# Performance work log

Measured on AMD Instinct MI355X. Metric: run time of the kernel, lower is better.

## Reference

```python
import jax, jax.numpy as jnp
import numpy as np

B, C, H, W = 32, 3, 128, 128
OH, OW = 32, 32
N = OH * OW


def calc_mask(mu_x, mu_y, sigma_x, sigma_y):
    # Gaussian receptive-field mask, normalized per neuron over (C,H,W) and
    # rescaled by sqrt(C*H*W), as in AdaptiveLocal2DLayer.calc_U (channel_separate=False,
    # normed=True). The mask is identical across channels, so we keep it [H,W,N]
    # and fold the channel count C into the normalization.
    xg = jnp.linspace(0.0, 1.0, W)
    yg = jnp.linspace(0.0, 1.0, H)
    gx = jnp.exp(-0.5 * ((xg[:, None] - mu_x[None, :]) / sigma_x[None, :]) ** 2)  # [W,N]
    gy = jnp.exp(-0.5 * ((yg[:, None] - mu_y[None, :]) / sigma_y[None, :]) ** 2)  # [H,N]
    g = gy[:, None, :] * gx[None, :, :]  # [H,W,N]
    sumsq = C * jnp.sum(g * g, axis=(0, 1), keepdims=True)  # per-neuron sum over C,H,W
    return g / jnp.sqrt(sumsq) * jnp.sqrt(jnp.asarray(C * H * W, dtype=g.dtype))


def setup_inputs() -> dict:
    key = jax.random.key(0)
    kx, kw = jax.random.split(key)
    x = jax.random.normal(kx, (B, C, H, W), dtype=jnp.float32)
    # mu_init='spread': grid of centers with margin 0.2 (np.meshgrid default 'xy')
    margin = 0.2
    grid_y, grid_x = jnp.meshgrid(
        jnp.linspace(margin, 1.0 - margin, OH),
        jnp.linspace(margin, 1.0 - margin, OW),
        indexing='xy')
    mu_x = grid_x.flatten().astype(jnp.float32)
    mu_y = grid_y.flatten().astype(jnp.float32)
    sigma_x = jnp.full((N,), 0.1, dtype=jnp.float32)
    sigma_y = jnp.full((N,), 0.1, dtype=jnp.float32)
    # weight init as in the module: uniform(-bound, bound) with
    # bound = gain*sqrt(6/(eff_fan_in + fan_out)), eff_fan_in = sum(mask^2)
    mask = calc_mask(mu_x, mu_y, sigma_x, sigma_y)
    eff_fan_in = C * jnp.sum(mask ** 2)
    gain = float(np.sqrt(2.0))  # calculate_gain('relu')
    bound = gain * jnp.sqrt(6.0 / (eff_fan_in + N))
    weights = jax.random.uniform(kw, (C, H, W, N), minval=-bound, maxval=bound,
                                 dtype=jnp.float32)
    return {"x": x, "mu_x": mu_x, "mu_y": mu_y,
            "sigma_x": sigma_x, "sigma_y": sigma_y, "weights": weights}


def reference(x, mu_x, mu_y, sigma_x, sigma_y, weights):
    # forward: weighted_mask = mask * weights; tensordot over (C,H,W)
    mask = calc_mask(mu_x, mu_y, sigma_x, sigma_y)  # [H,W,N]
    wm = mask[None, :, :, :] * weights               # [C,H,W,N]
    out = jnp.einsum('bchw,chwn->bn', x, wm)         # [B,N]
    return out.reshape(x.shape[0], 1, OH, OW)
```

## Files before the change

kernel.cpp:

```cpp
#include <hip/hip_runtime.h>

#define BB 32
#define CC 3
#define HH 128
#define WW 128
#define NN 1024
#define KK (CC*HH*WW)
#define NROWS (CC*HH)
#define KSR NROWS
#define BH 16
#define BSPLIT (BB/BH)
#define WCH 4
#define NCH (WW/WCH)
#define SG 8
#define STEP (1.0f/127.0f)

__global__ void scale_kernel(const float* __restrict__ mu_x,
                             const float* __restrict__ mu_y,
                             const float* __restrict__ sigma_x,
                             const float* __restrict__ sigma_y,
                             float* __restrict__ scale) {
    int n = blockIdx.x * blockDim.x + threadIdx.x;
    if (n >= NN) return;
    float mux = mu_x[n], muy = mu_y[n];
    float isx = 1.0f / sigma_x[n], isy = 1.0f / sigma_y[n];
    float Sx = 0.f, Sy = 0.f;
    for (int i = 0; i < WW; ++i) {
        float dx = (i * STEP - mux) * isx;
        Sx += __expf(-dx * dx);
        float dy = (i * STEP - muy) * isy;
        Sy += __expf(-dy * dy);
    }
    scale[n] = sqrtf((float)(HH * WW) / (Sx * Sy));
}

__global__ void xpose_kernel(const float* __restrict__ x, float* __restrict__ xT) {
    __shared__ float tile[64][BB + 1];
    int k0 = blockIdx.x * 64;
    int lane = threadIdx.x & 63;
    int bgrp = threadIdx.x >> 6;
#pragma unroll
    for (int i = 0; i < 8; ++i) {
        int b = bgrp * 8 + i;
        tile[lane][b] = x[(size_t)b * KK + k0 + lane];
    }
    __syncthreads();
    int b = threadIdx.x & 31;
    int kk0 = threadIdx.x >> 5;
#pragma unroll
    for (int i = 0; i < 8; ++i) {
        int kk = i * 8 + kk0;
        xT[(size_t)(k0 + kk) * BB + b] = tile[kk][b];
    }
}

__global__ __launch_bounds__(256) void main_pipe(
    const float* __restrict__ weights,
    const float* __restrict__ xT,
    const float* __restrict__ scale,
    const float* __restrict__ mu_x, const float* __restrict__ mu_y,
    const float* __restrict__ sigma_x, const float* __restrict__ sigma_y,
    float* __restrict__ part)
{
    const int tid  = threadIdx.x;
    const int wv   = tid >> 6;
    const int lane = tid & 63;

    const int d    = blockIdx.x;
    const int xcd  = d & 7;
    const int slot = d >> 3;
    const int g    = xcd * (KSR / 8) + (slot >> 1);
    const int b0   = (slot & 1) * BH;
    const int r    = g;
    const int h    = r & (HH - 1);
    const int nq   = wv * 64 + lane;

    const float4 mux = ((const float4*)mu_x)[nq];
    const float4 sx4 = ((const float4*)sigma_x)[nq];
    const float4 muy = ((const float4*)mu_y)[nq];
    const float4 sy4 = ((const float4*)sigma_y)[nq];
    const float4 sc4 = ((const float4*)scale)[nq];

    float4 ax, axs, Bf, gyrow;
    ax.x = -0.5f/(sx4.x*sx4.x); ax.y = -0.5f/(sx4.y*sx4.y);
    ax.z = -0.5f/(sx4.z*sx4.z); ax.w = -0.5f/(sx4.w*sx4.w);
    axs.x = ax.x*STEP; axs.y = ax.y*STEP; axs.z = ax.z*STEP; axs.w = ax.w*STEP;
    Bf.x = __expf(2.f*axs.x*STEP); Bf.y = __expf(2.f*axs.y*STEP);
    Bf.z = __expf(2.f*axs.z*STEP); Bf.w = __expf(2.f*axs.w*STEP);
    {
        const float hp = h * STEP;
        float ayc, dd;
        ayc = -0.5f/(sy4.x*sy4.x); dd = hp-muy.x; gyrow.x = __expf(ayc*dd*dd)*sc4.x;
        ayc = -0.5f/(sy4.y*sy4.y); dd = hp-muy.y; gyrow.y = __expf(ayc*dd*dd)*sc4.y;
        ayc = -0.5f/(sy4.z*sy4.z); dd = hp-muy.z; gyrow.z = __expf(ayc*dd*dd)*sc4.z;
        ayc = -0.5f/(sy4.w*sy4.w); dd = hp-muy.w; gyrow.w = __expf(ayc*dd*dd)*sc4.w;
    }

    const float* wbase = weights + (size_t)r * WW * NN + nq * 4;
    const float4* xr4  = (const float4*)xT + (size_t)r * (WW * BB / 4) + (b0 >> 2);

    float4 wR[2][4];
#define WLOAD(BUF, C)                                                   \
    {                                                                   \
        _Pragma("unroll")                                               \
        for (int i = 0; i < 4; ++i)                                     \
            wR[BUF][i] = *(const float4*)(wbase + (size_t)((C)*WCH + i) * NN); \
    }

    float4 acc[BH];
#pragma unroll
    for (int b = 0; b < BH; ++b) acc[b] = make_float4(0.f, 0.f, 0.f, 0.f);

    float4 g4, r4;
    auto resync = [&](int w0) {
        const float w0s = (float)w0 * STEP;
        float dd;
        dd = w0s - mux.x; g4.x = __expf(ax.x*dd*dd)*gyrow.x; r4.x = __expf(axs.x*(2.f*dd+STEP));
        dd = w0s - mux.y; g4.y = __expf(ax.y*dd*dd)*gyrow.y; r4.y = __expf(axs.y*(2.f*dd+STEP));
        dd = w0s - mux.z; g4.z = __expf(ax.z*dd*dd)*gyrow.z; r4.z = __expf(axs.z*(2.f*dd+STEP));
        dd = w0s - mux.w; g4.w = __expf(ax.w*dd*dd)*gyrow.w; r4.w = __expf(axs.w*(2.f*dd+STEP));
    };

#define FMAQ(XQ, A0)                                                    \
    {                                                                   \
        acc[A0+0].x = fmaf(XQ.x, t.x, acc[A0+0].x);                     \
        acc[A0+0].y = fmaf(XQ.x, t.y, acc[A0+0].y);                     \
        acc[A0+0].z = fmaf(XQ.x, t.z, acc[A0+0].z);                     \
        acc[A0+0].w = fmaf(XQ.x, t.w, acc[A0+0].w);                     \
        acc[A0+1].x = fmaf(XQ.y, t.x, acc[A0+1].x);                     \
        acc[A0+1].y = fmaf(XQ.y, t.y, acc[A0+1].y);                     \
        acc[A0+1].z = fmaf(XQ.y, t.z, acc[A0+1].z);                     \
        acc[A0+1].w = fmaf(XQ.y, t.w, acc[A0+1].w);                     \
        acc[A0+2].x = fmaf(XQ.z, t.x, acc[A0+2].x);                     \
        acc[A0+2].y = fmaf(XQ.z, t.y, acc[A0+2].y);                     \
        acc[A0+2].z = fmaf(XQ.z, t.z, acc[A0+2].z);                     \
        acc[A0+2].w = fmaf(XQ.z, t.w, acc[A0+2].w);                     \
        acc[A0+3].x = fmaf(XQ.w, t.x, acc[A0+3].x);                     \
        acc[A0+3].y = fmaf(XQ.w, t.y, acc[A0+3].y);                     \
        acc[A0+3].z = fmaf(XQ.w, t.z, acc[A0+3].z);                     \
        acc[A0+3].w = fmaf(XQ.w, t.w, acc[A0+3].w);                     \
    }

#define CHUNK(BUF, C)                                                   \
    {                                                                   \
        if (((C) & 3) == 0) resync((C) * WCH);                          \
        _Pragma("unroll")                                               \
        for (int i = 0; i < 4; ++i) {                                   \
            const int w = (C) * WCH + i;                                \
            const float4 xq0 = xr4[w*8 + 0];                            \
            const float4 xq1 = xr4[w*8 + 1];                            \
            const float4 xq2 = xr4[w*8 + 2];                            \
            const float4 xq3 = xr4[w*8 + 3];                            \
            const float4 wt  = wR[BUF][i];                              \
            float4 t;                                                   \
            t.x = g4.x * wt.x; t.y = g4.y * wt.y;                       \
            t.z = g4.z * wt.z; t.w = g4.w * wt.w;                       \
            FMAQ(xq0, 0)                                                \
            FMAQ(xq1, 4)                                                \
            FMAQ(xq2, 8)                                                \
            FMAQ(xq3, 12)                                               \
            g4.x *= r4.x; g4.y *= r4.y; g4.z *= r4.z; g4.w *= r4.w;     \
            r4.x *= Bf.x; r4.y *= Bf.y; r4.z *= Bf.z; r4.w *= Bf.w;     \
        }                                                               \
    }

    WLOAD(0, 0);
    for (int c = 0; c < NCH; c += 2) {
        WLOAD(1, c + 1);
        CHUNK(0, c);
        if (c + 2 < NCH) WLOAD(0, c + 2);
        CHUNK(1, c + 1);
    }
#undef CHUNK
#undef FMAQ
#undef WLOAD

    float* pp = part + ((size_t)g * BB + b0) * NN + (tid << 2);
#pragma unroll
    for (int b = 0; b < BH; ++b)
        *(float4*)(pp + (size_t)b * NN) = acc[b];
}

__global__ __launch_bounds__(256) void reduce1_kernel(const float* __restrict__ part,
                                                      float* __restrict__ part2) {
    const int sg = blockIdx.x >> 5;
    const int cq = (blockIdx.x & 31) * 256 + threadIdx.x;
    const int s0 = sg * (KSR / SG);
    float4 a = make_float4(0.f, 0.f, 0.f, 0.f);
#pragma unroll 4
    for (int s = 0; s < KSR / SG; ++s) {
        const float4 v = *(const float4*)(part + (size_t)(s0 + s) * (BB * NN) + cq * 4);
        a.x += v.x; a.y += v.y; a.z += v.z; a.w += v.w;
    }
    *(float4*)(part2 + ((size_t)sg * (BB * NN) + cq * 4)) = a;
}

__global__ __launch_bounds__(256) void reduce2_kernel(const float* __restrict__ part2,
                                                      float* __restrict__ out) {
    const int cq = blockIdx.x * 256 + threadIdx.x;
    float4 a = make_float4(0.f, 0.f, 0.f, 0.f);
#pragma unroll
    for (int sgi = 0; sgi < SG; ++sgi) {
        const float4 v = *(const float4*)(part2 + (size_t)sgi * (BB * NN) + cq * 4);
        a.x += v.x; a.y += v.y; a.z += v.z; a.w += v.w;
    }
    *(float4*)(out + cq * 4) = a;
}

__global__ __launch_bounds__(256) void main_fallback(
    const float* __restrict__ weights,
    const float* __restrict__ x,
    const float* __restrict__ mu_x, const float* __restrict__ mu_y,
    const float* __restrict__ sigma_x, const float* __restrict__ sigma_y,
    float* __restrict__ dst)
{
    __shared__ float tile[2][WW][8];
    const int tid = threadIdx.x;
    const int g   = blockIdx.x;
    const int b0  = blockIdx.y * 8;
    const int r0  = g * 2;

    {
        const int b = tid & 7;
        const int c = tid >> 3;
        const float* xp = x + (size_t)(b0 + b) * KK + (size_t)r0 * WW + c * 8;
        const float4 v0 = ((const float4*)xp)[0];
        const float4 v1 = ((const float4*)xp)[1];
        const int row = (c * 8) >> 7;
        const int w   = (c * 8) & (WW - 1);
        tile[row][w+0][b] = v0.x; tile[row][w+1][b] = v0.y;
        tile[row][w+2][b] = v0.z; tile[row][w+3][b] = v0.w;
        tile[row][w+4][b] = v1.x; tile[row][w+5][b] = v1.y;
        tile[row][w+6][b] = v1.z; tile[row][w+7][b] = v1.w;
    }

    float4 mux4 = ((const float4*)mu_x)[tid];
    float4 muy4 = ((const float4*)mu_y)[tid];
    float4 sx4  = ((const float4*)sigma_x)[tid];
    float4 sy4  = ((const float4*)sigma_y)[tid];
    float4 ax4, ay4, sc4;
    ax4.x=-0.5f/(sx4.x*sx4.x); ax4.y=-0.5f/(sx4.y*sx4.y);
    ax4.z=-0.5f/(sx4.z*sx4.z); ax4.w=-0.5f/(sx4.w*sx4.w);
    ay4.x=-0.5f/(sy4.x*sy4.x); ay4.y=-0.5f/(sy4.y*sy4.y);
    ay4.z=-0.5f/(sy4.z*sy4.z); ay4.w=-0.5f/(sy4.w*sy4.w);
    {
        float Sx[4]={0,0,0,0}, Sy[4]={0,0,0,0};
        for (int i = 0; i < WW; ++i) {
            float pp = i * STEP, dd;
            dd=pp-mux4.x; Sx[0]+=__expf(2.f*ax4.x*dd*dd);
            dd=pp-mux4.y; Sx[1]+=__expf(2.f*ax4.y*dd*dd);
            dd=pp-mux4.z; Sx[2]+=__expf(2.f*ax4.z*dd*dd);
            dd=pp-mux4.w; Sx[3]+=__expf(2.f*ax4.w*dd*dd);
            dd=pp-muy4.x; Sy[0]+=__expf(2.f*ay4.x*dd*dd);
            dd=pp-muy4.y; Sy[1]+=__expf(2.f*ay4.y*dd*dd);
            dd=pp-muy4.z; Sy[2]+=__expf(2.f*ay4.z*dd*dd);
            dd=pp-muy4.w; Sy[3]+=__expf(2.f*ay4.w*dd*dd);
        }
        sc4.x = sqrtf((float)(HH*WW)/(Sx[0]*Sy[0]));
        sc4.y = sqrtf((float)(HH*WW)/(Sx[1]*Sy[1]));
        sc4.z = sqrtf((float)(HH*WW)/(Sx[2]*Sy[2]));
        sc4.w = sqrtf((float)(HH*WW)/(Sx[3]*Sy[3]));
    }
    __syncthreads();

    float acc[8][4];
#pragma unroll
    for (int b = 0; b < 8; ++b)
        acc[b][0] = acc[b][1] = acc[b][2] = acc[b][3] = 0.f;

#pragma unroll
    for (int rr = 0; rr < 2; ++rr) {
        const int rrow = r0 + rr;
        const int hh = rrow & (HH - 1);
        float4 gys;
        {
            float hp = hh * STEP, dd;
            dd=hp-muy4.x; gys.x = __expf(ay4.x*dd*dd) * sc4.x;
            dd=hp-muy4.y; gys.y = __expf(ay4.y*dd*dd) * sc4.y;
            dd=hp-muy4.z; gys.z = __expf(ay4.z*dd*dd) * sc4.z;
            dd=hp-muy4.w; gys.w = __expf(ay4.w*dd*dd) * sc4.w;
        }
        const float4* wp = (const float4*)(weights + (size_t)rrow * WW * NN) + tid;
        float racc[8][4];
#pragma unroll
        for (int b = 0; b < 8; ++b)
            racc[b][0] = racc[b][1] = racc[b][2] = racc[b][3] = 0.f;
        for (int w = 0; w < WW; ++w) {
            const float4 wt = wp[(size_t)w * (NN/4)];
            float pp = w * STEP, dd;
            float4 t;
            dd=pp-mux4.x; t.x = __expf(ax4.x*dd*dd) * wt.x;
            dd=pp-mux4.y; t.y = __expf(ax4.y*dd*dd) * wt.y;
            dd=pp-mux4.z; t.z = __expf(ax4.z*dd*dd) * wt.z;
            dd=pp-mux4.w; t.w = __expf(ax4.w*dd*dd) * wt.w;
            const float4* trp = (const float4*)&tile[rr][w][0];
            float xs[8];
            ((float4*)xs)[0] = trp[0]; ((float4*)xs)[1] = trp[1];
#pragma unroll
            for (int b = 0; b < 8; ++b) {
                racc[b][0] = fmaf(xs[b], t.x, racc[b][0]);
                racc[b][1] = fmaf(xs[b], t.y, racc[b][1]);
                racc[b][2] = fmaf(xs[b], t.z, racc[b][2]);
                racc[b][3] = fmaf(xs[b], t.w, racc[b][3]);
            }
        }
#pragma unroll
        for (int b = 0; b < 8; ++b) {
            acc[b][0] = fmaf(gys.x, racc[b][0], acc[b][0]);
            acc[b][1] = fmaf(gys.y, racc[b][1], acc[b][1]);
            acc[b][2] = fmaf(gys.z, racc[b][2], acc[b][2]);
            acc[b][3] = fmaf(gys.w, racc[b][3], acc[b][3]);
        }
    }

    float* op = dst + (size_t)b0 * NN + tid * 4;
#pragma unroll
    for (int b = 0; b < 8; ++b) {
        atomicAdd(op + (size_t)b * NN + 0, acc[b][0]);
        atomicAdd(op + (size_t)b * NN + 1, acc[b][1]);
        atomicAdd(op + (size_t)b * NN + 2, acc[b][2]);
        atomicAdd(op + (size_t)b * NN + 3, acc[b][3]);
    }
}

extern "C" void kernel_launch(void* const* d_in, const int* in_sizes, int n_in,
                              void* d_out, int out_size, void* d_ws, size_t ws_size,
                              hipStream_t stream) {
    const float* x       = (const float*)d_in[0];
    const float* mu_x    = (const float*)d_in[1];
    const float* mu_y    = (const float*)d_in[2];
    const float* sigma_x = (const float*)d_in[3];
    const float* sigma_y = (const float*)d_in[4];
    const float* weights = (const float*)d_in[5];
    float* out = (float*)d_out;

    float* scale = (float*)d_ws;
    float* xT    = (float*)((char*)d_ws + 4096);
    float* part  = xT + (size_t)KK * BB;
    float* part2 = part + (size_t)KSR * BB * NN;
    const size_t need = 4096 +
        sizeof(float) * ((size_t)KK * BB + (size_t)KSR * BB * NN + (size_t)SG * BB * NN);

    if (ws_size >= need) {
        scale_kernel<<<(NN + 255) / 256, 256, 0, stream>>>(mu_x, mu_y, sigma_x, sigma_y, scale);
        xpose_kernel<<<KK / 64, 256, 0, stream>>>(x, xT);
        main_pipe<<<KSR * BSPLIT, 256, 0, stream>>>(weights, xT, scale,
                                                    mu_x, mu_y, sigma_x, sigma_y, part);
        reduce1_kernel<<<32 * SG, 256, 0, stream>>>(part, part2);
        reduce2_kernel<<<BB * NN / 4 / 256, 256, 0, stream>>>(part2, out);
    } else {
        hipMemsetAsync(d_out, 0, (size_t)out_size * sizeof(float), stream);
        dim3 grid(NROWS / 2, 4);
        main_fallback<<<grid, 256, 0, stream>>>(weights, x,
                                                mu_x, mu_y, sigma_x, sigma_y, out);
    }
}
```

Before: 74.23 us.

## Replace partial-sum buffer and two reduce kernels with direct atomicAdd accumulation

The main kernel now accumulates its per-row partial results straight into the zeroed output with float atomicAdd, removing the large partial buffer (384x32x1024 floats) and the two reduction kernels. To make the atomics coalesced, each thread now owns four strided neurons (stride 64) rather than four contiguous ones, so weight loads become scalar and lane-coalesced instead of float4. Batch order is rotated per row group to spread atomic contention. The cost is 384-way atomic contention per output element and a nondeterministic summation order.

```diff
diff --git a/kernel.cpp b/kernel.cpp
--- a/kernel.cpp
+++ b/kernel.cpp
@@ -12,7 +12,6 @@
 #define BSPLIT (BB/BH)
 #define WCH 4
 #define NCH (WW/WCH)
-#define SG 8
 #define STEP (1.0f/127.0f)
 
 __global__ void scale_kernel(const float* __restrict__ mu_x,
@@ -60,7 +59,7 @@
     const float* __restrict__ scale,
     const float* __restrict__ mu_x, const float* __restrict__ mu_y,
     const float* __restrict__ sigma_x, const float* __restrict__ sigma_y,
-    float* __restrict__ part)
+    float* __restrict__ out)
 {
     const int tid  = threadIdx.x;
     const int wv   = tid >> 6;
@@ -73,72 +72,63 @@
     const int b0   = (slot & 1) * BH;
     const int r    = g;
     const int h    = r & (HH - 1);
-    const int nq   = wv * 64 + lane;
-
-    const float4 mux = ((const float4*)mu_x)[nq];
-    const float4 sx4 = ((const float4*)sigma_x)[nq];
-    const float4 muy = ((const float4*)mu_y)[nq];
-    const float4 sy4 = ((const float4*)sigma_y)[nq];
-    const float4 sc4 = ((const float4*)scale)[nq];
-
-    float4 ax, axs, Bf, gyrow;
-    ax.x = -0.5f/(sx4.x*sx4.x); ax.y = -0.5f/(sx4.y*sx4.y);
-    ax.z = -0.5f/(sx4.z*sx4.z); ax.w = -0.5f/(sx4.w*sx4.w);
-    axs.x = ax.x*STEP; axs.y = ax.y*STEP; axs.z = ax.z*STEP; axs.w = ax.w*STEP;
-    Bf.x = __expf(2.f*axs.x*STEP); Bf.y = __expf(2.f*axs.y*STEP);
-    Bf.z = __expf(2.f*axs.z*STEP); Bf.w = __expf(2.f*axs.w*STEP);
-    {
-        const float hp = h * STEP;
-        float ayc, dd;
-        ayc = -0.5f/(sy4.x*sy4.x); dd = hp-muy.x; gyrow.x = __expf(ayc*dd*dd)*sc4.x;
-        ayc = -0.5f/(sy4.y*sy4.y); dd = hp-muy.y; gyrow.y = __expf(ayc*dd*dd)*sc4.y;
-        ayc = -0.5f/(sy4.z*sy4.z); dd = hp-muy.z; gyrow.z = __expf(ayc*dd*dd)*sc4.z;
-        ayc = -0.5f/(sy4.w*sy4.w); dd = hp-muy.w; gyrow.w = __expf(ayc*dd*dd)*sc4.w;
-    }
-
-    const float* wbase = weights + (size_t)r * WW * NN + nq * 4;
+    const int nbase = wv * 256 + lane;
+
+    float mux[4], ax[4], axs[4], Bf[4], gyrow[4];
+#pragma unroll
+    for (int j = 0; j < 4; ++j) {
+        const int n = nbase + j * 64;
+        const float mx  = mu_x[n];
+        const float sxv = sigma_x[n];
+        const float myv = mu_y[n];
+        const float syv = sigma_y[n];
+        const float scv = scale[n];
+        mux[j] = mx;
+        ax[j]  = -0.5f / (sxv * sxv);
+        axs[j] = ax[j] * STEP;
+        Bf[j]  = __expf(2.f * axs[j] * STEP);
+        const float ayc = -0.5f / (syv * syv);
+        const float dd  = h * STEP - myv;
+        gyrow[j] = __expf(ayc * dd * dd) * scv;
+    }
+
+    const float* wbase = weights + (size_t)r * WW * NN + nbase;
     const float4* xr4  = (const float4*)xT + (size_t)r * (WW * BB / 4) + (b0 >> 2);
 
-    float4 wR[2][4];
+    float wR[2][4][4];
 #define WLOAD(BUF, C)                                                   \
     {                                                                   \
         _Pragma("unroll")                                               \
-        for (int i = 0; i < 4; ++i)                                     \
-            wR[BUF][i] = *(const float4*)(wbase + (size_t)((C)*WCH + i) * NN); \
-    }
-
-    float4 acc[BH];
-#pragma unroll
-    for (int b = 0; b < BH; ++b) acc[b] = make_float4(0.f, 0.f, 0.f, 0.f);
-
-    float4 g4, r4;
+        for (int i = 0; i < 4; ++i) {                                   \
+            _Pragma("unroll")                                           \
+            for (int j = 0; j < 4; ++j)                                 \
+                wR[BUF][i][j] = wbase[(size_t)((C)*WCH + i) * NN + j * 64]; \
+        }                                                               \
+    }
+
+    float acc[BH][4];
+#pragma unroll
+    for (int b = 0; b < BH; ++b)
+#pragma unroll
+        for (int j = 0; j < 4; ++j) acc[b][j] = 0.f;
+
+    float g4[4], r4[4];
     auto resync = [&](int w0) {
         const float w0s = (float)w0 * STEP;
-        float dd;
-        dd = w0s - mux.x; g4.x = __expf(ax.x*dd*dd)*gyrow.x; r4.x = __expf(axs.x*(2.f*dd+STEP));
-        dd = w0s - mux.y; g4.y = __expf(ax.y*dd*dd)*gyrow.y; r4.y = __expf(axs.y*(2.f*dd+STEP));
-        dd = w0s - mux.z; g4.z = __expf(ax.z*dd*dd)*gyrow.z; r4.z = __expf(axs.z*(2.f*dd+STEP));
-        dd = w0s - mux.w; g4.w = __expf(ax.w*dd*dd)*gyrow.w; r4.w = __expf(axs.w*(2.f*dd+STEP));
+#pragma unroll
+        for (int j = 0; j < 4; ++j) {
+            const float dd = w0s - mux[j];
+            g4[j] = __expf(ax[j] * dd * dd) * gyrow[j];
+            r4[j] = __expf(axs[j] * (2.f * dd + STEP));
+        }
     };
 
-#define FMAQ(XQ, A0)                                                    \
+#define FMAQ(XC, B)                                                     \
     {                                                                   \
-        acc[A0+0].x = fmaf(XQ.x, t.x, acc[A0+0].x);                     \
-        acc[A0+0].y = fmaf(XQ.x, t.y, acc[A0+0].y);                     \
-        acc[A0+0].z = fmaf(XQ.x, t.z, acc[A0+0].z);                     \
-        acc[A0+0].w = fmaf(XQ.x, t.w, acc[A0+0].w);                     \
-        acc[A0+1].x = fmaf(XQ.y, t.x, acc[A0+1].x);                     \
-        acc[A0+1].y = fmaf(XQ.y, t.y, acc[A0+1].y);                     \
-        acc[A0+1].z = fmaf(XQ.y, t.z, acc[A0+1].z);                     \
-        acc[A0+1].w = fmaf(XQ.y, t.w, acc[A0+1].w);                     \
-        acc[A0+2].x = fmaf(XQ.z, t.x, acc[A0+2].x);                     \
-        acc[A0+2].y = fmaf(XQ.z, t.y, acc[A0+2].y);                     \
-        acc[A0+2].z = fmaf(XQ.z, t.z, acc[A0+2].z);                     \
-        acc[A0+2].w = fmaf(XQ.z, t.w, acc[A0+2].w);                     \
-        acc[A0+3].x = fmaf(XQ.w, t.x, acc[A0+3].x);                     \
-        acc[A0+3].y = fmaf(XQ.w, t.y, acc[A0+3].y);                     \
-        acc[A0+3].z = fmaf(XQ.w, t.z, acc[A0+3].z);                     \
-        acc[A0+3].w = fmaf(XQ.w, t.w, acc[A0+3].w);                     \
+        acc[B][0] = fmaf(XC, t0, acc[B][0]);                            \
+        acc[B][1] = fmaf(XC, t1, acc[B][1]);                            \
+        acc[B][2] = fmaf(XC, t2, acc[B][2]);                            \
+        acc[B][3] = fmaf(XC, t3, acc[B][3]);                            \
     }
 
 #define CHUNK(BUF, C)                                                   \
@@ -151,16 +141,16 @@
             const float4 xq1 = xr4[w*8 + 1];                            \
             const float4 xq2 = xr4[w*8 + 2];                            \
             const float4 xq3 = xr4[w*8 + 3];                            \
-            const float4 wt  = wR[BUF][i];                              \
-            float4 t;                                                   \
-            t.x = g4.x * wt.x; t.y = g4.y * wt.y;                       \
-            t.z = g4.z * wt.z; t.w = g4.w * wt.w;                       \
-            FMAQ(xq0, 0)                                                \
-            FMAQ(xq1, 4)                                                \
-            FMAQ(xq2, 8)                                                \
-            FMAQ(xq3, 12)                                               \
-            g4.x *= r4.x; g4.y *= r4.y; g4.z *= r4.z; g4.w *= r4.w;     \
-            r4.x *= Bf.x; r4.y *= Bf.y; r4.z *= Bf.z; r4.w *= Bf.w;     \
+            const float t0 = g4[0] * wR[BUF][i][0];                     \
+            const float t1 = g4[1] * wR[BUF][i][1];                     \
+            const float t2 = g4[2] * wR[BUF][i][2];                     \
+            const float t3 = g4[3] * wR[BUF][i][3];                     \
+            FMAQ(xq0.x,  0) FMAQ(xq0.y,  1) FMAQ(xq0.z,  2) FMAQ(xq0.w,  3) \
+            FMAQ(xq1.x,  4) FMAQ(xq1.y,  5) FMAQ(xq1.z,  6) FMAQ(xq1.w,  7) \
+            FMAQ(xq2.x,  8) FMAQ(xq2.y,  9) FMAQ(xq2.z, 10) FMAQ(xq2.w, 11) \
+            FMAQ(xq3.x, 12) FMAQ(xq3.y, 13) FMAQ(xq3.z, 14) FMAQ(xq3.w, 15) \
+            g4[0] *= r4[0]; g4[1] *= r4[1]; g4[2] *= r4[2]; g4[3] *= r4[3]; \
+            r4[0] *= Bf[0]; r4[1] *= Bf[1]; r4[2] *= Bf[2]; r4[3] *= Bf[3]; \
         }                                                               \
     }
 
@@ -175,36 +165,15 @@
 #undef FMAQ
 #undef WLOAD
 
-    float* pp = part + ((size_t)g * BB + b0) * NN + (tid << 2);
-#pragma unroll
-    for (int b = 0; b < BH; ++b)
-        *(float4*)(pp + (size_t)b * NN) = acc[b];
-}
-
-__global__ __launch_bounds__(256) void reduce1_kernel(const float* __restrict__ part,
-                                                      float* __restrict__ part2) {
-    const int sg = blockIdx.x >> 5;
-    const int cq = (blockIdx.x & 31) * 256 + threadIdx.x;
-    const int s0 = sg * (KSR / SG);
-    float4 a = make_float4(0.f, 0.f, 0.f, 0.f);
-#pragma unroll 4
-    for (int s = 0; s < KSR / SG; ++s) {
-        const float4 v = *(const float4*)(part + (size_t)(s0 + s) * (BB * NN) + cq * 4);
-        a.x += v.x; a.y += v.y; a.z += v.z; a.w += v.w;
-    }
-    *(float4*)(part2 + ((size_t)sg * (BB * NN) + cq * 4)) = a;
-}
-
-__global__ __launch_bounds__(256) void reduce2_kernel(const float* __restrict__ part2,
-                                                      float* __restrict__ out) {
-    const int cq = blockIdx.x * 256 + threadIdx.x;
-    float4 a = make_float4(0.f, 0.f, 0.f, 0.f);
-#pragma unroll
-    for (int sgi = 0; sgi < SG; ++sgi) {
-        const float4 v = *(const float4*)(part2 + (size_t)sgi * (BB * NN) + cq * 4);
-        a.x += v.x; a.y += v.y; a.z += v.z; a.w += v.w;
-    }
-    *(float4*)(out + cq * 4) = a;
+    const int rot = g & (BH - 1);
+#pragma unroll
+    for (int bb = 0; bb < BH; ++bb) {
+        const int b = (bb + rot) & (BH - 1);
+        float* op = out + (size_t)(b0 + b) * NN + nbase;
+#pragma unroll
+        for (int j = 0; j < 4; ++j)
+            atomicAdd(op + j * 64, acc[b][j]);
+    }
 }
 
 __global__ __launch_bounds__(256) void main_fallback(
@@ -336,20 +305,16 @@
 
     float* scale = (float*)d_ws;
     float* xT    = (float*)((char*)d_ws + 4096);
-    float* part  = xT + (size_t)KK * BB;
-    float* part2 = part + (size_t)KSR * BB * NN;
-    const size_t need = 4096 +
-        sizeof(float) * ((size_t)KK * BB + (size_t)KSR * BB * NN + (size_t)SG * BB * NN);
+    const size_t need = 4096 + sizeof(float) * (size_t)KK * BB;
+
+    hipMemsetAsync(d_out, 0, (size_t)out_size * sizeof(float), stream);
 
     if (ws_size >= need) {
         scale_kernel<<<(NN + 255) / 256, 256, 0, stream>>>(mu_x, mu_y, sigma_x, sigma_y, scale);
         xpose_kernel<<<KK / 64, 256, 0, stream>>>(x, xT);
         main_pipe<<<KSR * BSPLIT, 256, 0, stream>>>(weights, xT, scale,
-                                                    mu_x, mu_y, sigma_x, sigma_y, part);
-        reduce1_kernel<<<32 * SG, 256, 0, stream>>>(part, part2);
-        reduce2_kernel<<<BB * NN / 4 / 256, 256, 0, stream>>>(part2, out);
+                                                    mu_x, mu_y, sigma_x, sigma_y, out);
     } else {
-        hipMemsetAsync(d_out, 0, (size_t)out_size * sizeof(float), stream);
         dim3 grid(NROWS / 2, 4);
         main_fallback<<<grid, 256, 0, stream>>>(weights, x,
                                                 mu_x, mu_y, sigma_x, sigma_y, out);
```

New measurement: 99.32 us. +33.8%, slower.

## Split neuron dimension across two blocks, halving per-thread columns to float2

Applied to the files above, without the earlier changes.

Each main_pipe block now covers half of the N neurons, and each thread handles 2 neuron columns instead of 4. The grid doubles from KSR*2 to KSR*4 blocks. The intent is to halve accumulator registers (32 instead of 64), which should raise occupancy and give more parallelism to hide the latency of the weight stream. The cost is that each x value from xT is loaded twice as often relative to the FMAs done with it, and weight loads shrink to 8-byte accesses.

```diff
diff --git a/kernel.cpp b/kernel.cpp
--- a/kernel.cpp
+++ b/kernel.cpp
@@ -9,7 +9,7 @@
 #define NROWS (CC*HH)
 #define KSR NROWS
 #define BH 16
-#define BSPLIT (BB/BH)
+#define NSL 512
 #define WCH 4
 #define NCH (WW/WCH)
 #define SG 8
@@ -62,83 +62,67 @@
     const float* __restrict__ sigma_x, const float* __restrict__ sigma_y,
     float* __restrict__ part)
 {
-    const int tid  = threadIdx.x;
-    const int wv   = tid >> 6;
-    const int lane = tid & 63;
+    const int tid = threadIdx.x;
 
     const int d    = blockIdx.x;
     const int xcd  = d & 7;
     const int slot = d >> 3;
-    const int g    = xcd * (KSR / 8) + (slot >> 1);
-    const int b0   = (slot & 1) * BH;
+    const int g    = xcd * (KSR / 8) + (slot >> 2);
+    const int sib  = slot & 3;
+    const int b0   = (sib & 1) * BH;
+    const int nh   = sib >> 1;
     const int r    = g;
     const int h    = r & (HH - 1);
-    const int nq   = wv * 64 + lane;
-
-    const float4 mux = ((const float4*)mu_x)[nq];
-    const float4 sx4 = ((const float4*)sigma_x)[nq];
-    const float4 muy = ((const float4*)mu_y)[nq];
-    const float4 sy4 = ((const float4*)sigma_y)[nq];
-    const float4 sc4 = ((const float4*)scale)[nq];
-
-    float4 ax, axs, Bf, gyrow;
-    ax.x = -0.5f/(sx4.x*sx4.x); ax.y = -0.5f/(sx4.y*sx4.y);
-    ax.z = -0.5f/(sx4.z*sx4.z); ax.w = -0.5f/(sx4.w*sx4.w);
-    axs.x = ax.x*STEP; axs.y = ax.y*STEP; axs.z = ax.z*STEP; axs.w = ax.w*STEP;
-    Bf.x = __expf(2.f*axs.x*STEP); Bf.y = __expf(2.f*axs.y*STEP);
-    Bf.z = __expf(2.f*axs.z*STEP); Bf.w = __expf(2.f*axs.w*STEP);
+    const int np   = nh * 256 + tid;
+
+    const float2 mux2 = ((const float2*)mu_x)[np];
+    const float2 sx2  = ((const float2*)sigma_x)[np];
+    const float2 muy2 = ((const float2*)mu_y)[np];
+    const float2 sy2  = ((const float2*)sigma_y)[np];
+    const float2 sc2  = ((const float2*)scale)[np];
+
+    float mux[2] = {mux2.x, mux2.y};
+    float ax[2], axs[2], Bf[2], gyrow[2];
+    ax[0] = -0.5f/(sx2.x*sx2.x); ax[1] = -0.5f/(sx2.y*sx2.y);
+    axs[0] = ax[0]*STEP;         axs[1] = ax[1]*STEP;
+    Bf[0] = __expf(2.f*axs[0]*STEP); Bf[1] = __expf(2.f*axs[1]*STEP);
     {
         const float hp = h * STEP;
         float ayc, dd;
-        ayc = -0.5f/(sy4.x*sy4.x); dd = hp-muy.x; gyrow.x = __expf(ayc*dd*dd)*sc4.x;
-        ayc = -0.5f/(sy4.y*sy4.y); dd = hp-muy.y; gyrow.y = __expf(ayc*dd*dd)*sc4.y;
-        ayc = -0.5f/(sy4.z*sy4.z); dd = hp-muy.z; gyrow.z = __expf(ayc*dd*dd)*sc4.z;
-        ayc = -0.5f/(sy4.w*sy4.w); dd = hp-muy.w; gyrow.w = __expf(ayc*dd*dd)*sc4.w;
-    }
-
-    const float* wbase = weights + (size_t)r * WW * NN + nq * 4;
+        ayc = -0.5f/(sy2.x*sy2.x); dd = hp-muy2.x; gyrow[0] = __expf(ayc*dd*dd)*sc2.x;
+        ayc = -0.5f/(sy2.y*sy2.y); dd = hp-muy2.y; gyrow[1] = __expf(ayc*dd*dd)*sc2.y;
+    }
+
+    const float* wbase = weights + (size_t)r * WW * NN + np * 2;
     const float4* xr4  = (const float4*)xT + (size_t)r * (WW * BB / 4) + (b0 >> 2);
 
-    float4 wR[2][4];
+    float2 wR[2][4];
 #define WLOAD(BUF, C)                                                   \
     {                                                                   \
         _Pragma("unroll")                                               \
         for (int i = 0; i < 4; ++i)                                     \
-            wR[BUF][i] = *(const float4*)(wbase + (size_t)((C)*WCH + i) * NN); \
-    }
-
-    float4 acc[BH];
-#pragma unroll
-    for (int b = 0; b < BH; ++b) acc[b] = make_float4(0.f, 0.f, 0.f, 0.f);
-
-    float4 g4, r4;
+            wR[BUF][i] = *(const float2*)(wbase + (size_t)((C)*WCH + i) * NN); \
+    }
+
+    float2 acc[BH];
+#pragma unroll
+    for (int b = 0; b < BH; ++b) acc[b] = make_float2(0.f, 0.f);
+
+    float g2[2], r2[2];
     auto resync = [&](int w0) {
         const float w0s = (float)w0 * STEP;
-        float dd;
-        dd = w0s - mux.x; g4.x = __expf(ax.x*dd*dd)*gyrow.x; r4.x = __expf(axs.x*(2.f*dd+STEP));
-        dd = w0s - mux.y; g4.y = __expf(ax.y*dd*dd)*gyrow.y; r4.y = __expf(axs.y*(2.f*dd+STEP));
-        dd = w0s - mux.z; g4.z = __expf(ax.z*dd*dd)*gyrow.z; r4.z = __expf(axs.z*(2.f*dd+STEP));
-        dd = w0s - mux.w; g4.w = __expf(ax.w*dd*dd)*gyrow.w; r4.w = __expf(axs.w*(2.f*dd+STEP));
+#pragma unroll
+        for (int j = 0; j < 2; ++j) {
+            const float dd = w0s - mux[j];
+            g2[j] = __expf(ax[j] * dd * dd) * gyrow[j];
+            r2[j] = __expf(axs[j] * (2.f * dd + STEP));
+        }
     };
 
-#define FMAQ(XQ, A0)                                                    \
+#define FMAQ(XC, B)                                                     \
     {                                                                   \
-        acc[A0+0].x = fmaf(XQ.x, t.x, acc[A0+0].x);                     \
-        acc[A0+0].y = fmaf(XQ.x, t.y, acc[A0+0].y);                     \
-        acc[A0+0].z = fmaf(XQ.x, t.z, acc[A0+0].z);                     \
-        acc[A0+0].w = fmaf(XQ.x, t.w, acc[A0+0].w);                     \
-        acc[A0+1].x = fmaf(XQ.y, t.x, acc[A0+1].x);                     \
-        acc[A0+1].y = fmaf(XQ.y, t.y, acc[A0+1].y);                     \
-        acc[A0+1].z = fmaf(XQ.y, t.z, acc[A0+1].z);                     \
-        acc[A0+1].w = fmaf(XQ.y, t.w, acc[A0+1].w);                     \
-        acc[A0+2].x = fmaf(XQ.z, t.x, acc[A0+2].x);                     \
-        acc[A0+2].y = fmaf(XQ.z, t.y, acc[A0+2].y);                     \
-        acc[A0+2].z = fmaf(XQ.z, t.z, acc[A0+2].z);                     \
-        acc[A0+2].w = fmaf(XQ.z, t.w, acc[A0+2].w);                     \
-        acc[A0+3].x = fmaf(XQ.w, t.x, acc[A0+3].x);                     \
-        acc[A0+3].y = fmaf(XQ.w, t.y, acc[A0+3].y);                     \
-        acc[A0+3].z = fmaf(XQ.w, t.z, acc[A0+3].z);                     \
-        acc[A0+3].w = fmaf(XQ.w, t.w, acc[A0+3].w);                     \
+        acc[B].x = fmaf(XC, t0, acc[B].x);                              \
+        acc[B].y = fmaf(XC, t1, acc[B].y);                              \
     }
 
 #define CHUNK(BUF, C)                                                   \
@@ -151,16 +135,14 @@
             const float4 xq1 = xr4[w*8 + 1];                            \
             const float4 xq2 = xr4[w*8 + 2];                            \
             const float4 xq3 = xr4[w*8 + 3];                            \
-            const float4 wt  = wR[BUF][i];                              \
-            float4 t;                                                   \
-            t.x = g4.x * wt.x; t.y = g4.y * wt.y;                       \
-            t.z = g4.z * wt.z; t.w = g4.w * wt.w;                       \
-            FMAQ(xq0, 0)                                                \
-            FMAQ(xq1, 4)                                                \
-            FMAQ(xq2, 8)                                                \
-            FMAQ(xq3, 12)                                               \
-            g4.x *= r4.x; g4.y *= r4.y; g4.z *= r4.z; g4.w *= r4.w;     \
-            r4.x *= Bf.x; r4.y *= Bf.y; r4.z *= Bf.z; r4.w *= Bf.w;     \
+            const float t0 = g2[0] * wR[BUF][i].x;                      \
+            const float t1 = g2[1] * wR[BUF][i].y;                      \
+            FMAQ(xq0.x,  0) FMAQ(xq0.y,  1) FMAQ(xq0.z,  2) FMAQ(xq0.w,  3) \
+            FMAQ(xq1.x,  4) FMAQ(xq1.y,  5) FMAQ(xq1.z,  6) FMAQ(xq1.w,  7) \
+            FMAQ(xq2.x,  8) FMAQ(xq2.y,  9) FMAQ(xq2.z, 10) FMAQ(xq2.w, 11) \
+            FMAQ(xq3.x, 12) FMAQ(xq3.y, 13) FMAQ(xq3.z, 14) FMAQ(xq3.w, 15) \
+            g2[0] *= r2[0]; g2[1] *= r2[1];                             \
+            r2[0] *= Bf[0]; r2[1] *= Bf[1];                             \
         }                                                               \
     }
 
@@ -175,10 +157,10 @@
 #undef FMAQ
 #undef WLOAD
 
-    float* pp = part + ((size_t)g * BB + b0) * NN + (tid << 2);
+    float* pp = part + ((size_t)g * BB + b0) * NN + np * 2;
 #pragma unroll
     for (int b = 0; b < BH; ++b)
-        *(float4*)(pp + (size_t)b * NN) = acc[b];
+        *(float2*)(pp + (size_t)b * NN) = acc[b];
 }
 
 __global__ __launch_bounds__(256) void reduce1_kernel(const float* __restrict__ part,
@@ -344,8 +326,8 @@
     if (ws_size >= need) {
         scale_kernel<<<(NN + 255) / 256, 256, 0, stream>>>(mu_x, mu_y, sigma_x, sigma_y, scale);
         xpose_kernel<<<KK / 64, 256, 0, stream>>>(x, xT);
-        main_pipe<<<KSR * BSPLIT, 256, 0, stream>>>(weights, xT, scale,
-                                                    mu_x, mu_y, sigma_x, sigma_y, part);
+        main_pipe<<<KSR * 4, 256, 0, stream>>>(weights, xT, scale,
+                                               mu_x, mu_y, sigma_x, sigma_y, part);
         reduce1_kernel<<<32 * SG, 256, 0, stream>>>(part, part2);
         reduce2_kernel<<<BB * NN / 4 / 256, 256, 0, stream>>>(part2, out);
     } else {
```

After: 76.97 us. +3.7%, slower.
